# Optimization experiments

Hardware: AMD Instinct MI355X
Metric: run time of the kernel (lower is better)

Reference implementation:

```python
import jax, jax.numpy as jnp
import numpy as np

HEADS = 4  # opt['heads']; attention_dim=128 -> d_k=32


def setup_inputs() -> dict:
    key = jax.random.key(0)
    ks = jax.random.split(key, 8)
    N, E, IN_F, ATT = 50000, 1600000, 256, 128
    x = jax.random.normal(ks[0], (N, IN_F), dtype=jnp.float32)
    edge = jax.random.randint(ks[1], (2, E), 0, N, dtype=jnp.int64)
    Qw = jax.random.normal(ks[2], (ATT, IN_F), dtype=jnp.float32) * 0.02
    Qb = jax.random.normal(ks[3], (ATT,), dtype=jnp.float32) * 0.02
    Kw = jax.random.normal(ks[4], (ATT, IN_F), dtype=jnp.float32) * 0.02
    Kb = jax.random.normal(ks[5], (ATT,), dtype=jnp.float32) * 0.02
    Vw = jax.random.normal(ks[6], (ATT, IN_F), dtype=jnp.float32) * 0.02
    Vb = jax.random.normal(ks[7], (ATT,), dtype=jnp.float32) * 0.02
    return {"x": x, "edge": edge, "Qw": Qw, "Qb": Qb, "Kw": Kw, "Kb": Kb, "Vw": Vw, "Vb": Vb}


def reference(x, edge, Qw, Qb, Kw, Kb, Vw, Vb):
    N = x.shape[0]
    att = Qw.shape[0]
    d_k = att // HEADS
    inv_sqrt_dk = np.float32(1.0 / np.sqrt(d_k))
    # projections, split into heads: [N, h, d_k]
    q = (x @ Qw.T + Qb).reshape(N, HEADS, d_k)
    k = (x @ Kw.T + Kb).reshape(N, HEADS, d_k)
    v = (x @ Vw.T + Vb).reshape(N, HEADS, d_k)
    src, dst = edge[0], edge[1]
    # per-edge dot-product scores over d_k: [E, h]
    scores = jnp.einsum('ehd,ehd->eh', q[src], k[dst]) * inv_sqrt_dk
    # segment softmax grouped by source node (edge[0])
    m = jax.ops.segment_max(scores, src, num_segments=N)  # [N, h]
    ex = jnp.exp(scores - m[src])
    denom = jax.ops.segment_sum(ex, src, num_segments=N)  # [N, h]
    attn = ex / denom[src]  # [E, h]
    # spmm per head: out[src] += attn * v[dst]; fused over heads
    out = jax.ops.segment_sum(attn[:, :, None] * v[dst], src, num_segments=N)  # [N, h, d_k]
    # torch cat over heads == head-major flatten
    return out.reshape(N, att)
```

## Files before the change

### kernel.cpp

```cpp
#include <hip/hip_runtime.h>

#define HEADS 4
#define ATT   128
#define INF   256
#define DK    32
#define KVROW 384
#define BSTRIDE 10240

typedef __attribute__((ext_vector_type(8))) short bf16x8;
typedef __attribute__((ext_vector_type(4))) float f32x4;
typedef __attribute__((ext_vector_type(2))) float f32x2;

__device__ __forceinline__ unsigned short f2bf(float f) {
    unsigned u = __float_as_uint(f);
    unsigned r = u + 0x7fffu + ((u >> 16) & 1u);
    return (unsigned short)(r >> 16);
}

__device__ __forceinline__ unsigned char f2fp8(float f) {
    return (unsigned char)(__builtin_amdgcn_cvt_pk_fp8_f32(f, f, 0, false) & 0xff);
}

__device__ __forceinline__ void gload_lds16(const void* g, void* s) {
    __builtin_amdgcn_global_load_lds(
        (const __attribute__((address_space(1))) void*)g,
        (__attribute__((address_space(3))) void*)s,
        16, 0, 0);
}

__global__ void detect_kernel(const int* __restrict__ e32, int E, int* __restrict__ flag) {
    if (threadIdx.x == 0 && blockIdx.x == 0) {
        int allzero = 1;
        for (int i = 0; i < 256; ++i) {
            if (e32[2 * i + 1] != 0) { allzero = 0; break; }
        }
        *flag = allzero;
    }
}

__device__ __forceinline__ void load_edge(const int* __restrict__ e32, int is64, int E, int e,
                                          int& s, int& d) {
    if (is64) {
        s = e32[(size_t)2 * e];
        d = e32[(size_t)2 * ((size_t)E + e)];
    } else {
        s = e32[e];
        d = e32[(size_t)E + e];
    }
}

__global__ __launch_bounds__(256) void cast_kernel(const float* __restrict__ in,
                                                   unsigned short* __restrict__ out, int n8) {
    int stride = gridDim.x * 256;
    for (int i = blockIdx.x * 256 + threadIdx.x; i < n8; i += stride) {
        float4 a = ((const float4*)in)[(size_t)i * 2];
        float4 b = ((const float4*)in)[(size_t)i * 2 + 1];
        uint4 o;
        o.x = (unsigned)f2bf(a.x) | ((unsigned)f2bf(a.y) << 16);
        o.y = (unsigned)f2bf(a.z) | ((unsigned)f2bf(a.w) << 16);
        o.z = (unsigned)f2bf(b.x) | ((unsigned)f2bf(b.y) << 16);
        o.w = (unsigned)f2bf(b.z) | ((unsigned)f2bf(b.w) << 16);
        ((uint4*)out)[i] = o;
    }
}

__global__ __launch_bounds__(256) void cast3_kernel(const float* __restrict__ a,
                                                    const float* __restrict__ b,
                                                    const float* __restrict__ c,
                                                    unsigned short* __restrict__ out, int n8) {
    const float* in = (blockIdx.y == 0) ? a : (blockIdx.y == 1) ? b : c;
    unsigned short* o = out + (size_t)blockIdx.y * n8 * 8;
    int stride = gridDim.x * 256;
    for (int i = blockIdx.x * 256 + threadIdx.x; i < n8; i += stride) {
        float4 p = ((const float4*)in)[(size_t)i * 2];
        float4 q = ((const float4*)in)[(size_t)i * 2 + 1];
        uint4 w;
        w.x = (unsigned)f2bf(p.x) | ((unsigned)f2bf(p.y) << 16);
        w.y = (unsigned)f2bf(p.z) | ((unsigned)f2bf(p.w) << 16);
        w.z = (unsigned)f2bf(q.x) | ((unsigned)f2bf(q.y) << 16);
        w.w = (unsigned)f2bf(q.z) | ((unsigned)f2bf(q.w) << 16);
        ((uint4*)o)[i] = w;
    }
}

__global__ __launch_bounds__(256) void proj_mfma(
    const unsigned short* __restrict__ xb,
    const unsigned short* __restrict__ wb,
    const float* __restrict__ Bq, const float* __restrict__ Bk, const float* __restrict__ Bv,
    float* __restrict__ qout, unsigned char* __restrict__ kv, int N)
{
    __shared__ unsigned short As[128 * 32];
    __shared__ unsigned short Bs[128 * 32];

    const int t  = threadIdx.x;
    const int l  = t & 63;
    const int w  = t >> 6;
    const int wr = w >> 1, wc = w & 1;
    const int n0 = blockIdx.x * 128;
    const int mat = blockIdx.y;
    const unsigned short* W = wb + (size_t)mat * 128 * 256;

    f32x4 zero = {0.f, 0.f, 0.f, 0.f};
    f32x4 acc[4][4];
#pragma unroll
    for (int m = 0; m < 4; ++m)
#pragma unroll
        for (int n = 0; n < 4; ++n) acc[m][n] = zero;

    for (int k0 = 0; k0 < INF; k0 += 32) {
#pragma unroll
        for (int j = 0; j < 2; ++j) {
            int c = j * 256 + t;
            int row = c >> 2, part = c & 3;
            int gr = n0 + row; if (gr > N - 1) gr = N - 1;
            gload_lds16(xb + (size_t)gr * INF + k0 + part * 8,
                        &As[(size_t)(j * 256 + (w << 6)) * 8]);
        }
#pragma unroll
        for (int j = 0; j < 2; ++j) {
            int c = j * 256 + t;
            int row = c >> 2, part = c & 3;
            gload_lds16(W + (size_t)row * INF + k0 + part * 8,
                        &Bs[(size_t)(j * 256 + (w << 6)) * 8]);
        }
        __syncthreads();

        bf16x8 af[4], bfr[4];
#pragma unroll
        for (int m = 0; m < 4; ++m) {
            int row = wr * 64 + m * 16 + (l & 15);
            af[m] = *(const bf16x8*)&As[row * 32 + (l >> 4) * 8];
        }
#pragma unroll
        for (int n = 0; n < 4; ++n) {
            int row = wc * 64 + n * 16 + (l & 15);
            bfr[n] = *(const bf16x8*)&Bs[row * 32 + (l >> 4) * 8];
        }
#pragma unroll
        for (int m = 0; m < 4; ++m)
#pragma unroll
            for (int n = 0; n < 4; ++n)
                acc[m][n] = __builtin_amdgcn_mfma_f32_16x16x32_bf16(af[m], bfr[n], acc[m][n], 0, 0, 0);
        __syncthreads();
    }

    const float* bias = (mat == 0) ? Bq : ((mat == 1) ? Bk : Bv);

#pragma unroll
    for (int m = 0; m < 4; ++m) {
#pragma unroll
        for (int r = 0; r < 4; ++r) {
            int node = n0 + wr * 64 + m * 16 + (l >> 4) * 4 + r;
            if (node < N) {
                unsigned char* kvrow = kv + (size_t)node * KVROW;
#pragma unroll
                for (int n = 0; n < 4; ++n) {
                    int col = wc * 64 + n * 16 + (l & 15);
                    float val = acc[m][n][r] + bias[col];
                    if (mat == 0) {
                        qout[(size_t)node * ATT + col] = val;
                    } else if (mat == 1) {
                        kvrow[col] = f2fp8(val * 16.0f);
                    } else {
                        *(unsigned short*)(kvrow + 128 + col * 2) = f2bf(val);
                    }
                }
            }
        }
    }
}

#define PCHUNK 4096
__global__ __launch_bounds__(256) void partA_kernel(const int* __restrict__ e32,
                                                    const int* __restrict__ flag, int E,
                                                    int* __restrict__ gbcnt,
                                                    unsigned* __restrict__ eperm) {
    __shared__ int hist[256];
    __shared__ int lcur[256];
    const int t = threadIdx.x;
    const int base = blockIdx.x * PCHUNK;
    const int is64 = *flag;
    hist[t] = 0;
    __syncthreads();

    int s[16], d[16];
#pragma unroll
    for (int j = 0; j < 16; ++j) {
        int e = base + j * 256 + t;
        s[j] = -1; d[j] = 0;
        if (e < E) {
            load_edge(e32, is64, E, e, s[j], d[j]);
            atomicAdd(&hist[s[j] >> 8], 1);
        }
    }
    __syncthreads();
    int h = hist[t];
    int boff = 0;
    if (h > 0) boff = atomicAdd(&gbcnt[t], h);
    lcur[t] = t * BSTRIDE + boff;
    __syncthreads();
#pragma unroll
    for (int j = 0; j < 16; ++j) {
        if (s[j] >= 0) {
            int pos = atomicAdd(&lcur[s[j] >> 8], 1);
            eperm[pos] = ((unsigned)(s[j] & 255) << 16) | (unsigned)d[j];
        }
    }
}

__global__ __launch_bounds__(256) void partB_kernel(const unsigned* __restrict__ eperm,
                                                    const int* __restrict__ gbcnt,
                                                    uint2* __restrict__ off2,
                                                    int* __restrict__ sdst, int N) {
    __shared__ int hist[256];
    __shared__ int ws[4];
    __shared__ int lcur[256];
    const int b = blockIdx.x;
    const int t = threadIdx.x;
    const int lane = t & 63, w = t >> 6;
    const int base = b * BSTRIDE;
    const int cntb = gbcnt[b];

    hist[t] = 0;
    __syncthreads();
    for (int i = t; i < cntb; i += 256)
        atomicAdd(&hist[eperm[base + i] >> 16], 1);
    __syncthreads();

    int x = hist[t];
    int s = x;
#pragma unroll
    for (int d = 1; d < 64; d <<= 1) { int u = __shfl_up(s, d, 64); if (lane >= d) s += u; }
    if (lane == 63) ws[w] = s;
    __syncthreads();
    int carry = 0;
    for (int i = 0; i < w; ++i) carry += ws[i];
    int exc = carry + s - x;

    int node = (b << 8) + t;
    if (node < N) off2[node] = make_uint2((unsigned)(base + exc), (unsigned)(base + exc + x));
    lcur[t] = base + exc;
    __syncthreads();

    for (int i = t; i < cntb; i += 256) {
        unsigned p = eperm[base + i];
        int pos = atomicAdd(&lcur[p >> 16], 1);
        sdst[pos] = (int)(p & 0xffffu);
    }
}

__device__ __forceinline__ void pair_acc(unsigned kb, uint2 vv, bool live,
                                         float q0, float q1, float q2, float q3,
                                         float& o0, float& o1, float& o2, float& o3,
                                         float& den) {
    f32x2 k01 = __builtin_amdgcn_cvt_pk_f32_fp8((int)kb, false);
    f32x2 k23 = __builtin_amdgcn_cvt_pk_f32_fp8((int)kb, true);
    float part = fmaf(q0, k01[0], fmaf(q1, k01[1], fmaf(q2, k23[0], q3 * k23[1])));
    part += __shfl_xor(part, 1, 64);
    part += __shfl_xor(part, 2, 64);
    part += __shfl_xor(part, 4, 64);
    float p = live ? exp2f(part) : 0.f;
    den += p;
    float v0 = __uint_as_float(vv.x << 16);
    float v1 = __uint_as_float(vv.x & 0xffff0000u);
    float v2 = __uint_as_float(vv.y << 16);
    float v3 = __uint_as_float(vv.y & 0xffff0000u);
    o0 = fmaf(p, v0, o0);
    o1 = fmaf(p, v1, o1);
    o2 = fmaf(p, v2, o2);
    o3 = fmaf(p, v3, o3);
}

__global__ __launch_bounds__(256) void attn_kernel(
    const float* __restrict__ q, const unsigned char* __restrict__ kv,
    const uint2* __restrict__ off2, const int* __restrict__ sdst,
    float* __restrict__ out, int N)
{
    const int wid = blockIdx.x * 4 + (threadIdx.x >> 6);
    const int l = threadIdx.x & 63;
    if (wid >= N) return;
    const uint2 oo = off2[wid];
    const int e0 = (int)oo.x, e1 = (int)oo.y;
    const int half = l >> 5, sub = l & 31;

    const float sc2 = 0.17677669529663687f * 1.4426950408889634f / 16.0f;
    float4 q4 = *(const float4*)&q[(size_t)wid * ATT + sub * 4];
    float q0 = q4.x * sc2, q1 = q4.y * sc2, q2 = q4.z * sc2, q3 = q4.w * sc2;
    float o0 = 0.f, o1 = 0.f, o2 = 0.f, o3 = 0.f, den = 0.f;

    for (int base = e0; base < e1; base += 64) {
        int cnt = e1 - base; if (cnt > 64) cnt = 64;
        int dl = sdst[base + (l < cnt ? l : cnt - 1)];
        int j = 0;
        for (; j + 8 <= cnt; j += 8) {
            int d0 = __shfl(dl, j + half, 64);
            int d1 = __shfl(dl, j + 2 + half, 64);
            int d2 = __shfl(dl, j + 4 + half, 64);
            int d3 = __shfl(dl, j + 6 + half, 64);
            const unsigned char* r0 = kv + (size_t)d0 * KVROW;
            const unsigned char* r1 = kv + (size_t)d1 * KVROW;
            const unsigned char* r2 = kv + (size_t)d2 * KVROW;
            const unsigned char* r3 = kv + (size_t)d3 * KVROW;
            unsigned kb0 = *(const unsigned*)(r0 + sub * 4);
            uint2    vv0 = *(const uint2*)(r0 + 128 + sub * 8);
            unsigned kb1 = *(const unsigned*)(r1 + sub * 4);
            uint2    vv1 = *(const uint2*)(r1 + 128 + sub * 8);
            unsigned kb2 = *(const unsigned*)(r2 + sub * 4);
            uint2    vv2 = *(const uint2*)(r2 + 128 + sub * 8);
            unsigned kb3 = *(const unsigned*)(r3 + sub * 4);
            uint2    vv3 = *(const uint2*)(r3 + 128 + sub * 8);
            pair_acc(kb0, vv0, true, q0, q1, q2, q3, o0, o1, o2, o3, den);
            pair_acc(kb1, vv1, true, q0, q1, q2, q3, o0, o1, o2, o3, den);
            pair_acc(kb2, vv2, true, q0, q1, q2, q3, o0, o1, o2, o3, den);
            pair_acc(kb3, vv3, true, q0, q1, q2, q3, o0, o1, o2, o3, den);
        }
        for (; j + 4 <= cnt; j += 4) {
            int d0 = __shfl(dl, j + half, 64);
            int d1 = __shfl(dl, j + 2 + half, 64);
            const unsigned char* r0 = kv + (size_t)d0 * KVROW;
            const unsigned char* r1 = kv + (size_t)d1 * KVROW;
            unsigned kb0 = *(const unsigned*)(r0 + sub * 4);
            uint2    vv0 = *(const uint2*)(r0 + 128 + sub * 8);
            unsigned kb1 = *(const unsigned*)(r1 + sub * 4);
            uint2    vv1 = *(const uint2*)(r1 + 128 + sub * 8);
            pair_acc(kb0, vv0, true, q0, q1, q2, q3, o0, o1, o2, o3, den);
            pair_acc(kb1, vv1, true, q0, q1, q2, q3, o0, o1, o2, o3, den);
        }
        for (; j < cnt; j += 2) {
            int jj = j + half;
            int da = __shfl(dl, jj, 64);
            const unsigned char* r0 = kv + (size_t)da * KVROW;
            unsigned kb0 = *(const unsigned*)(r0 + sub * 4);
            uint2    vv0 = *(const uint2*)(r0 + 128 + sub * 8);
            pair_acc(kb0, vv0, jj < cnt, q0, q1, q2, q3, o0, o1, o2, o3, den);
        }
    }
    den += __shfl_xor(den, 32, 64);
    o0 += __shfl_xor(o0, 32, 64);
    o1 += __shfl_xor(o1, 32, 64);
    o2 += __shfl_xor(o2, 32, 64);
    o3 += __shfl_xor(o3, 32, 64);
    float r = (den > 0.f) ? 1.0f / den : 0.f;
    if (half == 0)
        *(float4*)&out[(size_t)wid * ATT + sub * 4] =
            make_float4(o0 * r, o1 * r, o2 * r, o3 * r);
}

extern "C" void kernel_launch(void* const* d_in, const int* in_sizes, int n_in,
                              void* d_out, int out_size, void* d_ws, size_t ws_size,
                              hipStream_t stream)
{
    const float* x   = (const float*)d_in[0];
    const int*   e32 = (const int*)d_in[1];
    const float* Wq  = (const float*)d_in[2];
    const float* Bq  = (const float*)d_in[3];
    const float* Wk  = (const float*)d_in[4];
    const float* Bk  = (const float*)d_in[5];
    const float* Wv  = (const float*)d_in[6];
    const float* Bv  = (const float*)d_in[7];
    float* out = (float*)d_out;

    const int N = in_sizes[0] / INF;
    const int E = in_sizes[1] / 2;

    char* ws = (char*)d_ws;
    size_t o = 0;
    auto take = [&](size_t bytes) -> char* {
        char* p = ws + o;
        o = (o + bytes + 255) & ~(size_t)255;
        return p;
    };
    unsigned short* xb = (unsigned short*)take((size_t)N * INF * 2);
    unsigned short* wb = (unsigned short*)take((size_t)3 * ATT * INF * 2);
    float*          q  = (float*)take((size_t)N * ATT * 4);
    unsigned char*  kv = (unsigned char*)take((size_t)N * KVROW);
    uint2* off2  = (uint2*)take((size_t)N * 8);
    int*   gbcnt = (int*)take(1024);
    unsigned* eperm = (unsigned*)take((size_t)256 * BSTRIDE * 4);
    int*   sdst  = (int*)take((size_t)256 * BSTRIDE * 4);
    int*   flag  = (int*)take(4);
    (void)ws_size; (void)n_in; (void)out_size;

    const int nb = (N + 255) / 256;

    detect_kernel<<<1, 64, 0, stream>>>(e32, E, flag);
    (void)hipMemsetAsync(gbcnt, 0, 1024, stream);

    cast_kernel<<<2048, 256, 0, stream>>>(x, xb, N * (INF / 8));
    cast3_kernel<<<dim3(16, 3), 256, 0, stream>>>(Wq, Wk, Wv, wb, (ATT * INF) / 8);

    proj_mfma<<<dim3((N + 127) / 128, 3), 256, 0, stream>>>(xb, wb, Bq, Bk, Bv, q, kv, N);

    partA_kernel<<<(E + PCHUNK - 1) / PCHUNK, 256, 0, stream>>>(e32, flag, E, gbcnt, eperm);
    partB_kernel<<<nb, 256, 0, stream>>>(eperm, gbcnt, off2, sdst, N);

    attn_kernel<<<(N + 3) / 4, 256, 0, stream>>>(q, kv, off2, sdst, out, N);
}
```

Baseline: 184.6 us.

## Fuse x cast into projection, store Q as bf16, inline int64 detection

Drops the separate fp32-to-bf16 cast kernel for x and converts x to bf16 inside the projection GEMM's tile load, replacing async global-to-LDS loads with register loads, conversion and LDS stores. Q is now stored as bf16, halving the Q traffic written by the projection and read by the attention kernel. The detect kernel is removed; each partition block checks the edge dtype itself and uses 16-byte vector loads on the int64 path. This cuts launches and memory traffic, but the projection re-reads fp32 x three times (once per matrix) and Q loses precision.

```diff
diff --git a/kernel.cpp b/kernel.cpp
--- a/kernel.cpp
+++ b/kernel.cpp
@@ -26,42 +26,6 @@
         (const __attribute__((address_space(1))) void*)g,
         (__attribute__((address_space(3))) void*)s,
         16, 0, 0);
-}
-
-__global__ void detect_kernel(const int* __restrict__ e32, int E, int* __restrict__ flag) {
-    if (threadIdx.x == 0 && blockIdx.x == 0) {
-        int allzero = 1;
-        for (int i = 0; i < 256; ++i) {
-            if (e32[2 * i + 1] != 0) { allzero = 0; break; }
-        }
-        *flag = allzero;
-    }
-}
-
-__device__ __forceinline__ void load_edge(const int* __restrict__ e32, int is64, int E, int e,
-                                          int& s, int& d) {
-    if (is64) {
-        s = e32[(size_t)2 * e];
-        d = e32[(size_t)2 * ((size_t)E + e)];
-    } else {
-        s = e32[e];
-        d = e32[(size_t)E + e];
-    }
-}
-
-__global__ __launch_bounds__(256) void cast_kernel(const float* __restrict__ in,
-                                                   unsigned short* __restrict__ out, int n8) {
-    int stride = gridDim.x * 256;
-    for (int i = blockIdx.x * 256 + threadIdx.x; i < n8; i += stride) {
-        float4 a = ((const float4*)in)[(size_t)i * 2];
-        float4 b = ((const float4*)in)[(size_t)i * 2 + 1];
-        uint4 o;
-        o.x = (unsigned)f2bf(a.x) | ((unsigned)f2bf(a.y) << 16);
-        o.y = (unsigned)f2bf(a.z) | ((unsigned)f2bf(a.w) << 16);
-        o.z = (unsigned)f2bf(b.x) | ((unsigned)f2bf(b.y) << 16);
-        o.w = (unsigned)f2bf(b.z) | ((unsigned)f2bf(b.w) << 16);
-        ((uint4*)out)[i] = o;
-    }
 }
 
 __global__ __launch_bounds__(256) void cast3_kernel(const float* __restrict__ a,
@@ -84,10 +48,10 @@
 }
 
 __global__ __launch_bounds__(256) void proj_mfma(
-    const unsigned short* __restrict__ xb,
+    const float* __restrict__ x,
     const unsigned short* __restrict__ wb,
     const float* __restrict__ Bq, const float* __restrict__ Bk, const float* __restrict__ Bv,
-    float* __restrict__ qout, unsigned char* __restrict__ kv, int N)
+    unsigned short* __restrict__ qout, unsigned char* __restrict__ kv, int N)
 {
     __shared__ unsigned short As[128 * 32];
     __shared__ unsigned short Bs[128 * 32];
@@ -113,8 +77,14 @@
             int c = j * 256 + t;
             int row = c >> 2, part = c & 3;
             int gr = n0 + row; if (gr > N - 1) gr = N - 1;
-            gload_lds16(xb + (size_t)gr * INF + k0 + part * 8,
-                        &As[(size_t)(j * 256 + (w << 6)) * 8]);
+            const float4* xp = (const float4*)&x[(size_t)gr * INF + k0 + part * 8];
+            float4 a = xp[0], b = xp[1];
+            uint4 o;
+            o.x = (unsigned)f2bf(a.x) | ((unsigned)f2bf(a.y) << 16);
+            o.y = (unsigned)f2bf(a.z) | ((unsigned)f2bf(a.w) << 16);
+            o.z = (unsigned)f2bf(b.x) | ((unsigned)f2bf(b.y) << 16);
+            o.w = (unsigned)f2bf(b.z) | ((unsigned)f2bf(b.w) << 16);
+            *(uint4*)&As[(size_t)c * 8] = o;
         }
 #pragma unroll
         for (int j = 0; j < 2; ++j) {
@@ -158,7 +128,7 @@
                     int col = wc * 64 + n * 16 + (l & 15);
                     float val = acc[m][n][r] + bias[col];
                     if (mat == 0) {
-                        qout[(size_t)node * ATT + col] = val;
+                        qout[(size_t)node * ATT + col] = f2bf(val);
                     } else if (mat == 1) {
                         kvrow[col] = f2fp8(val * 16.0f);
                     } else {
@@ -171,28 +141,49 @@
 }
 
 #define PCHUNK 4096
-__global__ __launch_bounds__(256) void partA_kernel(const int* __restrict__ e32,
-                                                    const int* __restrict__ flag, int E,
+__global__ __launch_bounds__(256) void partA_kernel(const int* __restrict__ e32, int E,
                                                     int* __restrict__ gbcnt,
                                                     unsigned* __restrict__ eperm) {
     __shared__ int hist[256];
     __shared__ int lcur[256];
+    __shared__ int s_is64;
     const int t = threadIdx.x;
     const int base = blockIdx.x * PCHUNK;
-    const int is64 = *flag;
+
+    if (t == 0) s_is64 = 1;
     hist[t] = 0;
     __syncthreads();
+    if (e32[2 * t + 1] != 0) s_is64 = 0;
+    __syncthreads();
+    const int is64 = s_is64;
 
     int s[16], d[16];
-#pragma unroll
-    for (int j = 0; j < 16; ++j) {
-        int e = base + j * 256 + t;
-        s[j] = -1; d[j] = 0;
-        if (e < E) {
-            load_edge(e32, is64, E, e, s[j], d[j]);
-            atomicAdd(&hist[s[j] >> 8], 1);
-        }
-    }
+    if (is64) {
+#pragma unroll
+        for (int j = 0; j < 8; ++j) {
+            int e2 = base + j * 512 + 2 * t;
+            s[2 * j] = -1; s[2 * j + 1] = -1; d[2 * j] = 0; d[2 * j + 1] = 0;
+            if (e2 + 1 < E) {
+                uint4 us = *(const uint4*)&e32[(size_t)2 * e2];
+                uint4 ud = *(const uint4*)&e32[(size_t)2 * ((size_t)E + e2)];
+                s[2 * j] = (int)us.x; d[2 * j] = (int)ud.x;
+                s[2 * j + 1] = (int)us.z; d[2 * j + 1] = (int)ud.z;
+            } else if (e2 < E) {
+                s[2 * j] = e32[(size_t)2 * e2];
+                d[2 * j] = e32[(size_t)2 * ((size_t)E + e2)];
+            }
+        }
+    } else {
+#pragma unroll
+        for (int j = 0; j < 16; ++j) {
+            int e = base + j * 256 + t;
+            s[j] = -1; d[j] = 0;
+            if (e < E) { s[j] = e32[e]; d[j] = e32[(size_t)E + e]; }
+        }
+    }
+#pragma unroll
+    for (int j = 0; j < 16; ++j)
+        if (s[j] >= 0) atomicAdd(&hist[s[j] >> 8], 1);
     __syncthreads();
     int h = hist[t];
     int boff = 0;
@@ -272,7 +263,7 @@
 }
 
 __global__ __launch_bounds__(256) void attn_kernel(
-    const float* __restrict__ q, const unsigned char* __restrict__ kv,
+    const unsigned short* __restrict__ qb, const unsigned char* __restrict__ kv,
     const uint2* __restrict__ off2, const int* __restrict__ sdst,
     float* __restrict__ out, int N)
 {
@@ -284,8 +275,11 @@
     const int half = l >> 5, sub = l & 31;
 
     const float sc2 = 0.17677669529663687f * 1.4426950408889634f / 16.0f;
-    float4 q4 = *(const float4*)&q[(size_t)wid * ATT + sub * 4];
-    float q0 = q4.x * sc2, q1 = q4.y * sc2, q2 = q4.z * sc2, q3 = q4.w * sc2;
+    uint2 qw = *(const uint2*)&qb[(size_t)wid * ATT + sub * 4];
+    float q0 = __uint_as_float(qw.x << 16) * sc2;
+    float q1 = __uint_as_float(qw.x & 0xffff0000u) * sc2;
+    float q2 = __uint_as_float(qw.y << 16) * sc2;
+    float q3 = __uint_as_float(qw.y & 0xffff0000u) * sc2;
     float o0 = 0.f, o1 = 0.f, o2 = 0.f, o3 = 0.f, den = 0.f;
 
     for (int base = e0; base < e1; base += 64) {
@@ -370,29 +364,24 @@
         o = (o + bytes + 255) & ~(size_t)255;
         return p;
     };
-    unsigned short* xb = (unsigned short*)take((size_t)N * INF * 2);
     unsigned short* wb = (unsigned short*)take((size_t)3 * ATT * INF * 2);
-    float*          q  = (float*)take((size_t)N * ATT * 4);
+    unsigned short* qb = (unsigned short*)take((size_t)N * ATT * 2);
     unsigned char*  kv = (unsigned char*)take((size_t)N * KVROW);
     uint2* off2  = (uint2*)take((size_t)N * 8);
     int*   gbcnt = (int*)take(1024);
     unsigned* eperm = (unsigned*)take((size_t)256 * BSTRIDE * 4);
     int*   sdst  = (int*)take((size_t)256 * BSTRIDE * 4);
-    int*   flag  = (int*)take(4);
     (void)ws_size; (void)n_in; (void)out_size;
 
     const int nb = (N + 255) / 256;
 
-    detect_kernel<<<1, 64, 0, stream>>>(e32, E, flag);
     (void)hipMemsetAsync(gbcnt, 0, 1024, stream);
-
-    cast_kernel<<<2048, 256, 0, stream>>>(x, xb, N * (INF / 8));
     cast3_kernel<<<dim3(16, 3), 256, 0, stream>>>(Wq, Wk, Wv, wb, (ATT * INF) / 8);
 
-    proj_mfma<<<dim3((N + 127) / 128, 3), 256, 0, stream>>>(xb, wb, Bq, Bk, Bv, q, kv, N);
-
-    partA_kernel<<<(E + PCHUNK - 1) / PCHUNK, 256, 0, stream>>>(e32, flag, E, gbcnt, eperm);
+    proj_mfma<<<dim3((N + 127) / 128, 3), 256, 0, stream>>>(x, wb, Bq, Bk, Bv, qb, kv, N);
+
+    partA_kernel<<<(E + PCHUNK - 1) / PCHUNK, 256, 0, stream>>>(e32, E, gbcnt, eperm);
     partB_kernel<<<nb, 256, 0, stream>>>(eperm, gbcnt, off2, sdst, N);
 
-    attn_kernel<<<(N + 3) / 4, 256, 0, stream>>>(q, kv, off2, sdst, out, N);
-}
+    attn_kernel<<<(N + 3) / 4, 256, 0, stream>>>(qb, kv, off2, sdst, out, N);
+}
```

Measured after the change: 177.2 us. -4.0%, faster.
